# Kernel tuning notes

Hardware: AMD Instinct MI355X
Metric: run time of the kernel (lower is better)

Reference implementation:

```python
import jax, jax.numpy as jnp
import numpy as np

WIN = 25  # win_size (odd) -> AvgPool1d preserves time length
PAD = (WIN - 1) // 2

def _avg_pool_same(xc):
    xp = jnp.pad(xc, ((0, 0), (0, 0), (PAD, PAD)))
    cs = jnp.cumsum(xp, axis=-1)
    zero = jnp.zeros(cs.shape[:-1] + (1,), cs.dtype)
    cs = jnp.concatenate([zero, cs], axis=-1)
    win_sum = cs[..., WIN:] - cs[..., :-WIN]  # [b, c, time]
    return win_sum / WIN

def setup_inputs() -> dict:
    key = jax.random.key(0)
    ks = jax.random.split(key, 5)
    B, S, C, P = 64, 720, 321, 336
    scale = 1.0 / np.sqrt(S)  # mimic nn.Linear init scale
    return {
        "x": jax.random.normal(ks[0], (B, S, C), jnp.float32),
        "W_res": jax.random.uniform(ks[1], (C, P, S), jnp.float32, -scale, scale),
        "b_res": jax.random.uniform(ks[2], (C, P), jnp.float32, -scale, scale),
        "W_trend": jax.random.uniform(ks[3], (C, P, S), jnp.float32, -scale, scale),
        "b_trend": jax.random.uniform(ks[4], (C, P), jnp.float32, -scale, scale),
    }

def reference(x, W_res, b_res, W_trend, b_trend):
    # x: [batch, seq_len, channel] -> [batch, channel, seq_len]
    xc = jnp.transpose(x, (0, 2, 1))
    season = _avg_pool_same(xc)            # trend (called 'mean' in torch code)
    res = xc - season
    # Per-channel Linear loop fused as one batched matmul over channels.
    res_out = jnp.einsum('bcs,cps->bcp', res, W_res) + b_res[None]
    trend_out = jnp.einsum('bcs,cps->bcp', season, W_trend) + b_trend[None]
    return res_out + trend_out  # [batch, channel, pred_len]
```

## Files before the change

### kernel.cpp

```cpp
#include <hip/hip_runtime.h>
#include <hip/hip_bf16.h>

#define B_ 64
#define S_ 720
#define C_ 321
#define P_ 336
#define SP 736
#define WIN 25
#define PADW 12
#define NTILE 112
#define KSTEPS 23

typedef __bf16 bf16x8 __attribute__((ext_vector_type(8)));
typedef float f32x4 __attribute__((ext_vector_type(4)));

__device__ __forceinline__ unsigned short f2bf(float f) {
  unsigned int u = __builtin_bit_cast(unsigned int, f);
  u += 0x7FFFu + ((u >> 16) & 1u);
  return (unsigned short)(u >> 16);
}

__global__ __launch_bounds__(256) void pass0_decomp(
    const float* __restrict__ x,
    ushort2* __restrict__ resT,
    ushort2* __restrict__ seaT) {
  __shared__ float xpad[S_ + 2 * PADW];
  int blk = blockIdx.x;
  int b = blk / C_;
  int c = blk - b * C_;
  int t = threadIdx.x;
  for (int s = t; s < S_; s += 256) xpad[PADW + s] = x[(b * S_ + s) * C_ + c];
  if (t < PADW) { xpad[t] = 0.f; xpad[PADW + S_ + t] = 0.f; }
  __syncthreads();
  int rowbase = (c * B_ + b) * (SP / 2);
  for (int p = t; p < SP / 2; p += 256) {
    if (p < S_ / 2) {
      int s0 = 2 * p;
      float w0 = 0.f;
#pragma unroll
      for (int j = 0; j < WIN; ++j) w0 += xpad[s0 + j];
      float w1 = w0 - xpad[s0] + xpad[s0 + WIN];
      float sea0 = w0 * (1.0f / WIN), sea1 = w1 * (1.0f / WIN);
      float x0 = xpad[PADW + s0], x1 = xpad[PADW + s0 + 1];
      resT[rowbase + p] = make_ushort2(f2bf(x0 - sea0), f2bf(x1 - sea1));
      seaT[rowbase + p] = make_ushort2(f2bf(sea0), f2bf(sea1));
    } else {
      resT[rowbase + p] = make_ushort2(0, 0);
      seaT[rowbase + p] = make_ushort2(0, 0);
    }
  }
}

__global__ __launch_bounds__(256) void gemm_fused(
    const uint4* __restrict__ abase,
    const float4* __restrict__ wR,
    const float4* __restrict__ wT,
    const float* __restrict__ bR,
    const float* __restrict__ bT,
    float* __restrict__ out) {
  __shared__ __align__(16) unsigned char lds[8192 + 14336 + 448];
  unsigned char* ldsA = lds;
  unsigned char* ldsB = lds + 8192;
  float* bsum = (float*)(lds + 8192 + 14336);

  int blk = blockIdx.x;
  int c = blk / 3;
  int nt = blk - c * 3;
  int p0 = nt * NTILE;
  int t = threadIdx.x;
  int w = t >> 6;
  int lane = t & 63;
  int col = lane & 15;
  int quad = lane >> 4;

  if (t < NTILE) bsum[t] = bR[c * P_ + p0 + t] + bT[c * P_ + p0 + t];

  int aOffG[2], aOffL[2];
#pragma unroll
  for (int i = 0; i < 2; ++i) {
    int idx = i * 256 + t;
    int m = idx >> 8;
    int r = (idx >> 2) & 63;
    int k16 = idx & 3;
    aOffG[i] = m * 1890048 + c * 5888 + r * 92 + k16;
    aOffL[i] = m * 4096 + r * 64 + k16 * 16;
  }
  int bOffG[7], bOffL[7], bK4[7], bM[7];
#pragma unroll
  for (int i = 0; i < 7; ++i) {
    int idx = i * 256 + t;
    int m = idx / 896;
    int rem = idx - m * 896;
    int r = rem >> 3;
    int k4 = rem & 7;
    bM[i] = m;
    bK4[i] = k4;
    bOffG[i] = c * 60480 + (p0 + r) * 180 + k4;
    bOffL[i] = m * 7168 + r * 64 + k4 * 8;
  }

  f32x4 acc[7];
#pragma unroll
  for (int i = 0; i < 7; ++i) acc[i] = (f32x4){0.f, 0.f, 0.f, 0.f};

  int aFragOff = (w * 16 + col) * 64 + quad * 16;

  for (int ks = 0; ks < KSTEPS; ++ks) {
    uint4 av[2];
#pragma unroll
    for (int i = 0; i < 2; ++i) av[i] = abase[aOffG[i] + ks * 4];
    float4 bv[7];
#pragma unroll
    for (int i = 0; i < 7; ++i) {
      float4 v = {0.f, 0.f, 0.f, 0.f};
      if (ks * 32 + bK4[i] * 4 < S_) {
        const float4* src = bM[i] ? wT : wR;
        v = src[bOffG[i] + ks * 8];
      }
      bv[i] = v;
    }
    __syncthreads();
#pragma unroll
    for (int i = 0; i < 2; ++i) *(uint4*)(ldsA + aOffL[i]) = av[i];
#pragma unroll
    for (int i = 0; i < 7; ++i) {
      ushort4 pk;
      pk.x = f2bf(bv[i].x); pk.y = f2bf(bv[i].y);
      pk.z = f2bf(bv[i].z); pk.w = f2bf(bv[i].w);
      *(ushort4*)(ldsB + bOffL[i]) = pk;
    }
    __syncthreads();
    bf16x8 aR = *(const bf16x8*)(ldsA + aFragOff);
    bf16x8 aS = *(const bf16x8*)(ldsA + 4096 + aFragOff);
#pragma unroll
    for (int tt = 0; tt < 7; ++tt) {
      int bo = (tt * 16 + col) * 64 + quad * 16;
      bf16x8 bRf = *(const bf16x8*)(ldsB + bo);
      bf16x8 bTf = *(const bf16x8*)(ldsB + 7168 + bo);
      acc[tt] = __builtin_amdgcn_mfma_f32_16x16x32_bf16(aR, bRf, acc[tt], 0, 0, 0);
      acc[tt] = __builtin_amdgcn_mfma_f32_16x16x32_bf16(aS, bTf, acc[tt], 0, 0, 0);
    }
  }

#pragma unroll
  for (int tt = 0; tt < 7; ++tt) {
    int p = p0 + tt * 16 + col;
    float bs = bsum[tt * 16 + col];
#pragma unroll
    for (int r = 0; r < 4; ++r) {
      int brow = w * 16 + quad * 4 + r;
      out[(brow * C_ + c) * P_ + p] = acc[tt][r] + bs;
    }
  }
}

extern "C" void kernel_launch(void* const* d_in, const int* in_sizes, int n_in,
                              void* d_out, int out_size, void* d_ws, size_t ws_size,
                              hipStream_t stream) {
  const float* x = (const float*)d_in[0];
  const float4* wR = (const float4*)d_in[1];
  const float* bR = (const float*)d_in[2];
  const float4* wT = (const float4*)d_in[3];
  const float* bT = (const float*)d_in[4];
  float* out = (float*)d_out;

  ushort2* resT = (ushort2*)d_ws;
  ushort2* seaT = resT + (size_t)C_ * B_ * (SP / 2);

  pass0_decomp<<<B_ * C_, 256, 0, stream>>>(x, resT, seaT);
  gemm_fused<<<C_ * 3, 256, 0, stream>>>((const uint4*)d_ws, wR, wT, bR, bT, out);
}
```

Before: 787.7 us.

## Tile decomposition over channels, pad LDS rows, and prefetch next k-step in GEMM

The decomposition kernel now handles 8 channels per block, so the strided reads of x become partially coalesced. It computes the moving average with a sliding-window running sum, stages the bf16 output in LDS and writes it out as 16-byte vectors. The GEMM pads LDS rows from 64 to 80 bytes to cut bank conflicts on fragment reads. It also register-prefetches the next k-step's global loads so they overlap the MFMA work, at the cost of more registers and LDS.

```diff
diff --git a/kernel.cpp b/kernel.cpp
--- a/kernel.cpp
+++ b/kernel.cpp
@@ -10,6 +10,8 @@
 #define PADW 12
 #define NTILE 112
 #define KSTEPS 23
+#define CT 8
+#define AQ_PER_MAT 1890048
 
 typedef __bf16 bf16x8 __attribute__((ext_vector_type(8)));
 typedef float f32x4 __attribute__((ext_vector_type(4)));
@@ -22,31 +24,56 @@
 
 __global__ __launch_bounds__(256) void pass0_decomp(
     const float* __restrict__ x,
-    ushort2* __restrict__ resT,
-    ushort2* __restrict__ seaT) {
-  __shared__ float xpad[S_ + 2 * PADW];
-  int blk = blockIdx.x;
-  int b = blk / C_;
-  int c = blk - b * C_;
+    uint4* __restrict__ resQ,
+    uint4* __restrict__ seaQ) {
+  __shared__ float xs[CT][745];
+  __shared__ unsigned short obuf[2 * CT * SP];
+  int c0 = blockIdx.x * CT;
+  int b = blockIdx.y;
   int t = threadIdx.x;
-  for (int s = t; s < S_; s += 256) xpad[PADW + s] = x[(b * S_ + s) * C_ + c];
-  if (t < PADW) { xpad[t] = 0.f; xpad[PADW + S_ + t] = 0.f; }
+
+  if (t < CT * 24) {
+    int c = t / 24, h = t % 24;
+    xs[c][h < 12 ? h : h + 720] = 0.f;
+  }
+  {
+    int m = t >> 7, c = (t >> 4) & 7, s = 720 + (t & 15);
+    obuf[(m * CT + c) * SP + s] = 0;
+  }
+  {
+    int c = t & 7;
+    int svalid = (c0 + c < C_);
+    for (int p = 0; p < 23; ++p) {
+      int s = (t >> 3) + p * 32;
+      if (s < S_ && svalid) xs[c][PADW + s] = x[(b * S_ + s) * C_ + c0 + c];
+    }
+  }
   __syncthreads();
-  int rowbase = (c * B_ + b) * (SP / 2);
-  for (int p = t; p < SP / 2; p += 256) {
-    if (p < S_ / 2) {
-      int s0 = 2 * p;
-      float w0 = 0.f;
-#pragma unroll
-      for (int j = 0; j < WIN; ++j) w0 += xpad[s0 + j];
-      float w1 = w0 - xpad[s0] + xpad[s0 + WIN];
-      float sea0 = w0 * (1.0f / WIN), sea1 = w1 * (1.0f / WIN);
-      float x0 = xpad[PADW + s0], x1 = xpad[PADW + s0 + 1];
-      resT[rowbase + p] = make_ushort2(f2bf(x0 - sea0), f2bf(x1 - sea1));
-      seaT[rowbase + p] = make_ushort2(f2bf(sea0), f2bf(sea1));
-    } else {
-      resT[rowbase + p] = make_ushort2(0, 0);
-      seaT[rowbase + p] = make_ushort2(0, 0);
+  {
+    int c = t & 7;
+    int s0 = (t >> 3) * 23;
+    int s1 = s0 + 23; if (s1 > S_) s1 = S_;
+    float wsum = 0.f;
+#pragma unroll
+    for (int j = 0; j < WIN; ++j) wsum += xs[c][s0 + j];
+    for (int s = s0; s < s1; ++s) {
+      float sea = wsum * (1.0f / WIN);
+      float res = xs[c][s + PADW] - sea;
+      obuf[c * SP + s] = f2bf(res);
+      obuf[(CT + c) * SP + s] = f2bf(sea);
+      wsum += xs[c][s + WIN] - xs[c][s];
+    }
+  }
+  __syncthreads();
+  const uint4* ob = (const uint4*)obuf;
+  for (int i = t; i < 2 * CT * 92; i += 256) {
+    int row = i / 92;
+    int off = i - row * 92;
+    int c = row & 7;
+    int m = row >> 3;
+    if (c0 + c < C_) {
+      uint4* dst = m ? seaQ : resQ;
+      dst[((c0 + c) * B_ + b) * 92 + off] = ob[row * 92 + off];
     }
   }
 }
@@ -58,10 +85,10 @@
     const float* __restrict__ bR,
     const float* __restrict__ bT,
     float* __restrict__ out) {
-  __shared__ __align__(16) unsigned char lds[8192 + 14336 + 448];
+  __shared__ __align__(16) unsigned char lds[10240 + 17920 + 448];
   unsigned char* ldsA = lds;
-  unsigned char* ldsB = lds + 8192;
-  float* bsum = (float*)(lds + 8192 + 14336);
+  unsigned char* ldsB = lds + 10240;
+  float* bsum = (float*)(lds + 10240 + 17920);
 
   int blk = blockIdx.x;
   int c = blk / 3;
@@ -82,8 +109,8 @@
     int m = idx >> 8;
     int r = (idx >> 2) & 63;
     int k16 = idx & 3;
-    aOffG[i] = m * 1890048 + c * 5888 + r * 92 + k16;
-    aOffL[i] = m * 4096 + r * 64 + k16 * 16;
+    aOffG[i] = m * AQ_PER_MAT + c * 5888 + r * 92 + k16;
+    aOffL[i] = m * 5120 + r * 80 + k16 * 16;
   }
   int bOffG[7], bOffL[7], bK4[7], bM[7];
 #pragma unroll
@@ -96,29 +123,30 @@
     bM[i] = m;
     bK4[i] = k4;
     bOffG[i] = c * 60480 + (p0 + r) * 180 + k4;
-    bOffL[i] = m * 7168 + r * 64 + k4 * 8;
+    bOffL[i] = m * 8960 + r * 80 + k4 * 8;
   }
 
   f32x4 acc[7];
 #pragma unroll
   for (int i = 0; i < 7; ++i) acc[i] = (f32x4){0.f, 0.f, 0.f, 0.f};
 
-  int aFragOff = (w * 16 + col) * 64 + quad * 16;
+  int aFragOff = (w * 16 + col) * 80 + quad * 16;
+
+  uint4 av[2];
+  float4 bv[7];
+#pragma unroll
+  for (int i = 0; i < 2; ++i) av[i] = abase[aOffG[i]];
+#pragma unroll
+  for (int i = 0; i < 7; ++i) {
+    float4 v = {0.f, 0.f, 0.f, 0.f};
+    if (bK4[i] * 4 < S_) {
+      const float4* src = bM[i] ? wT : wR;
+      v = src[bOffG[i]];
+    }
+    bv[i] = v;
+  }
 
   for (int ks = 0; ks < KSTEPS; ++ks) {
-    uint4 av[2];
-#pragma unroll
-    for (int i = 0; i < 2; ++i) av[i] = abase[aOffG[i] + ks * 4];
-    float4 bv[7];
-#pragma unroll
-    for (int i = 0; i < 7; ++i) {
-      float4 v = {0.f, 0.f, 0.f, 0.f};
-      if (ks * 32 + bK4[i] * 4 < S_) {
-        const float4* src = bM[i] ? wT : wR;
-        v = src[bOffG[i] + ks * 8];
-      }
-      bv[i] = v;
-    }
     __syncthreads();
 #pragma unroll
     for (int i = 0; i < 2; ++i) *(uint4*)(ldsA + aOffL[i]) = av[i];
@@ -130,26 +158,39 @@
       *(ushort4*)(ldsB + bOffL[i]) = pk;
     }
     __syncthreads();
+    if (ks + 1 < KSTEPS) {
+      int kn = ks + 1;
+#pragma unroll
+      for (int i = 0; i < 2; ++i) av[i] = abase[aOffG[i] + kn * 4];
+#pragma unroll
+      for (int i = 0; i < 7; ++i) {
+        float4 v = {0.f, 0.f, 0.f, 0.f};
+        if (kn * 32 + bK4[i] * 4 < S_) {
+          const float4* src = bM[i] ? wT : wR;
+          v = src[bOffG[i] + kn * 8];
+        }
+        bv[i] = v;
+      }
+    }
     bf16x8 aR = *(const bf16x8*)(ldsA + aFragOff);
-    bf16x8 aS = *(const bf16x8*)(ldsA + 4096 + aFragOff);
+    bf16x8 aS = *(const bf16x8*)(ldsA + 5120 + aFragOff);
 #pragma unroll
     for (int tt = 0; tt < 7; ++tt) {
-      int bo = (tt * 16 + col) * 64 + quad * 16;
+      int bo = (tt * 16 + col) * 80 + quad * 16;
       bf16x8 bRf = *(const bf16x8*)(ldsB + bo);
-      bf16x8 bTf = *(const bf16x8*)(ldsB + 7168 + bo);
+      bf16x8 bTf = *(const bf16x8*)(ldsB + 8960 + bo);
       acc[tt] = __builtin_amdgcn_mfma_f32_16x16x32_bf16(aR, bRf, acc[tt], 0, 0, 0);
       acc[tt] = __builtin_amdgcn_mfma_f32_16x16x32_bf16(aS, bTf, acc[tt], 0, 0, 0);
     }
   }
 
 #pragma unroll
-  for (int tt = 0; tt < 7; ++tt) {
-    int p = p0 + tt * 16 + col;
-    float bs = bsum[tt * 16 + col];
-#pragma unroll
-    for (int r = 0; r < 4; ++r) {
-      int brow = w * 16 + quad * 4 + r;
-      out[(brow * C_ + c) * P_ + p] = acc[tt][r] + bs;
+  for (int r = 0; r < 4; ++r) {
+    int brow = w * 16 + quad * 4 + r;
+#pragma unroll
+    for (int tt = 0; tt < 7; ++tt) {
+      int p = p0 + tt * 16 + col;
+      out[(brow * C_ + c) * P_ + p] = acc[tt][r] + bsum[tt * 16 + col];
     }
   }
 }
@@ -164,9 +205,10 @@
   const float* bT = (const float*)d_in[4];
   float* out = (float*)d_out;
 
-  ushort2* resT = (ushort2*)d_ws;
-  ushort2* seaT = resT + (size_t)C_ * B_ * (SP / 2);
-
-  pass0_decomp<<<B_ * C_, 256, 0, stream>>>(x, resT, seaT);
+  uint4* resQ = (uint4*)d_ws;
+  uint4* seaQ = resQ + AQ_PER_MAT;
+
+  dim3 g0((C_ + CT - 1) / CT, B_);
+  pass0_decomp<<<g0, 256, 0, stream>>>(x, resQ, seaQ);
   gemm_fused<<<C_ * 3, 256, 0, stream>>>((const uint4*)d_ws, wR, wT, bR, bT, out);
 }
```

Result: faster. 748.6 us (-5.0%).
